# Kernel optimization log

Measured on AMD Instinct MI355X. Metric: run time of the kernel, lower is better.

Reference implementation:

```python
import jax, jax.numpy as jnp
import numpy as np

K = 5            # trend_kernel_size
PAD = K // 2
EPS = 1e-5

def _ricker(k):
    # Ricker (mexican-hat) wavelet used as the Peaks kernel
    a = k / 4.0
    t = np.arange(k, dtype=np.float64) - (k - 1) / 2.0
    A = 2.0 / (np.sqrt(3.0 * a) * np.pi ** 0.25)
    return (A * (1.0 - (t / a) ** 2) * np.exp(-t ** 2 / (2.0 * a ** 2))).astype(np.float32)

def _ramp(k):
    # centered linear ramp -> local slope estimator for the Trend kernel
    return (np.linspace(-1.0, 1.0, k) / k).astype(np.float32)

_PEAK_W = jnp.asarray(_ricker(K))
_RAMP_W = jnp.asarray(_ramp(K))

def tconv(x, w):
    # 'same'-padded cross-correlation along the time axis (axis=2) of (B,C,T,H,W)
    T = x.shape[2]
    xp = jnp.pad(x, ((0, 0), (0, 0), (PAD, PAD), (0, 0), (0, 0)))
    out = w[0] * jax.lax.dynamic_slice_in_dim(xp, 0, T, axis=2)
    for j in range(1, K):
        out = out + w[j] * jax.lax.dynamic_slice_in_dim(xp, j, T, axis=2)
    return out

def bn(x, gamma, beta, axes):
    # training-mode batch norm over `axes`, channel axis = 1
    m = x.mean(axes, keepdims=True)
    v = x.var(axes, keepdims=True)
    xn = (x - m) * jax.lax.rsqrt(v + EPS)
    shp = [1] * x.ndim
    shp[1] = -1
    return xn * gamma.reshape(shp) + beta.reshape(shp)


def setup_inputs() -> dict:
    key = jax.random.key(0)
    ks = jax.random.split(key, 8)
    B, C, T, H, W = 4, 3, 12, 256, 256
    CH0 = 32
    return {
        'x':      jax.random.normal(ks[0], (B, C, T, H, W), jnp.float32),
        'w0':     jax.random.normal(ks[1], (CH0, C), jnp.float32) * 0.1,
        'g0':     jnp.ones((CH0,), jnp.float32),
        'b0':     jnp.zeros((CH0,), jnp.float32),
        'wrt':    jax.random.normal(ks[2], (1, CH0), jnp.float32) * 0.1,
        'grt':    jnp.ones((1,), jnp.float32),
        'brt':    jnp.zeros((1,), jnp.float32),
        'wtt':    jax.random.normal(ks[3], (1, C), jnp.float32) * 0.1,
        'gtt':    jnp.ones((1,), jnp.float32),
        'btt':    jnp.zeros((1,), jnp.float32),
        'w_th':   jax.random.normal(ks[4], (CH0, T), jnp.float32) * 0.1,
        'b_th':   jnp.zeros((CH0,), jnp.float32),
        'g_min':  jnp.ones((CH0,), jnp.float32),
        'b_min':  jnp.zeros((CH0,), jnp.float32),
        'g_max':  jnp.ones((CH0,), jnp.float32),
        'b_max':  jnp.zeros((CH0,), jnp.float32),
        'g_mean': jnp.ones((CH0,), jnp.float32),
        'b_mean': jnp.zeros((CH0,), jnp.float32),
    }


def reference(x, w0, g0, b0, wrt, grt, brt, wtt, gtt, btt,
              w_th, b_th, g_min, b_min, g_max, b_max, g_mean, b_mean):
    act = jax.nn.silu
    # --- per-band temporal kernels (vectorized over all bands/pixels) ---
    peak = tconv(x, _PEAK_W)                       # Peaks: ricker wavelet
    slope = tconv(x, _RAMP_W)                      # Trend: local slope
    trend = peak + jax.nn.relu(slope) + jax.nn.relu(-slope)  # (B,C,T,H,W)
    # --- time_conv0: 1x1x1 conv3d + BN3d + act ---
    h = act(bn(jnp.einsum('bcthw,oc->bothw', x, w0), g0, b0, (0, 2, 3, 4)))  # (B,32,T,H,W)
    # --- reduce_to_time / reduce_trend_to_time: 1x1x1 conv3d to 1 channel ---
    rt = act(bn(jnp.einsum('bcthw,oc->bothw', h, wrt), grt, brt, (0, 2, 3, 4)))[:, 0]      # (B,T,H,W)
    tt = act(bn(jnp.einsum('bcthw,oc->bothw', trend, wtt), gtt, btt, (0, 2, 3, 4)))[:, 0]  # (B,T,H,W)
    # --- time_to_hidden: 1x1 conv2d over the time-as-channels axis ---
    time_logits = jnp.einsum('bthw,ot->bohw', rt + tt, w_th) + b_th[None, :, None, None]
    # --- channel reductions over time + BN2d + act (mean branch uses max, as in source) ---
    xmin = h.min(axis=2)
    xmax = h.max(axis=2)
    cmin = act(bn(xmin, g_min, b_min, (0, 2, 3)))
    cmax = act(bn(xmax, g_max, b_max, (0, 2, 3)))
    cmean = act(bn(xmax, g_mean, b_mean, (0, 2, 3)))
    enc = time_logits + cmin + cmax + cmean        # (B,32,H,W)
    # --- InstanceNorm2d(affine=False) ---
    m = enc.mean((2, 3), keepdims=True)
    v = enc.var((2, 3), keepdims=True)
    return (enc - m) * jax.lax.rsqrt(v + EPS)
```

## Files before the change

kernel.cpp:

```cpp
#include <hip/hip_runtime.h>
#include <math.h>

#define HW_    65536
#define THW_   786432
#define NP     262144
#define N1_    3145728.0
#define N3_    262144.0

#define XB 0
#define SB 72
#define EB 1128
#define DWN 2152

__device__ __constant__ float PW_[5] = {-0.33647654f, 0.20279402f, 0.77575913f, 0.20279402f, -0.33647654f};
__device__ __constant__ float RW_[5] = {-0.2f, -0.1f, 0.0f, 0.1f, 0.2f};

typedef __fp16 fp16x2 __attribute__((ext_vector_type(2)));
union H2U { fp16x2 h; unsigned int u; };
__device__ __forceinline__ unsigned int packh(float a, float b) {
  H2U x; x.h = __builtin_amdgcn_cvt_pkrtz(a, b); return x.u;
}
__device__ __forceinline__ float2 unpackh(unsigned int v) {
  H2U x; x.u = v; return make_float2((float)x.h.x, (float)x.h.y);
}
__device__ __forceinline__ unsigned short pack1h(float a) {
  return (unsigned short)(packh(a, 0.f) & 0xffffu);
}

__device__ __forceinline__ float wred64(float v) {
#pragma unroll
  for (int m = 32; m > 0; m >>= 1) v += __shfl_xor(v, m, 64);
  return v;
}

__device__ __forceinline__ float fsilu(float y) {
  float e = __expf(-y);
  return y * __builtin_amdgcn_rcpf(1.0f + e);
}

__global__ __launch_bounds__(256) void k_xstats(const float* __restrict__ x, double* __restrict__ dws) {
  const int v = blockIdx.x * 256 + threadIdx.x;
  const float4* x4 = (const float4*)x;
  float s0 = 0, s1 = 0, s2 = 0, p00 = 0, p01 = 0, p02 = 0, p11 = 0, p12 = 0, p22 = 0;
#pragma unroll
  for (int b = 0; b < 4; b++) {
    float4 a0 = x4[(size_t)(b * 3 + 0) * 196608 + v];
    float4 a1 = x4[(size_t)(b * 3 + 1) * 196608 + v];
    float4 a2 = x4[(size_t)(b * 3 + 2) * 196608 + v];
    s0 += a0.x + a0.y + a0.z + a0.w;
    s1 += a1.x + a1.y + a1.z + a1.w;
    s2 += a2.x + a2.y + a2.z + a2.w;
    p00 += a0.x * a0.x + a0.y * a0.y + a0.z * a0.z + a0.w * a0.w;
    p11 += a1.x * a1.x + a1.y * a1.y + a1.z * a1.z + a1.w * a1.w;
    p22 += a2.x * a2.x + a2.y * a2.y + a2.z * a2.z + a2.w * a2.w;
    p01 += a0.x * a1.x + a0.y * a1.y + a0.z * a1.z + a0.w * a1.w;
    p02 += a0.x * a2.x + a0.y * a2.y + a0.z * a2.z + a0.w * a2.w;
    p12 += a1.x * a2.x + a1.y * a2.y + a1.z * a2.z + a1.w * a2.w;
  }
  float vals[9] = {s0, s1, s2, p00, p01, p02, p11, p12, p22};
  __shared__ float red[4][9];
  int wave = threadIdx.x >> 6, lane = threadIdx.x & 63;
#pragma unroll
  for (int q = 0; q < 9; q++) vals[q] = wred64(vals[q]);
  if (lane == 0) {
#pragma unroll
    for (int q = 0; q < 9; q++) red[wave][q] = vals[q];
  }
  __syncthreads();
  if (threadIdx.x < 9) {
    double t = (double)red[0][threadIdx.x] + red[1][threadIdx.x] + red[2][threadIdx.x] + red[3][threadIdx.x];
    atomicAdd(&dws[XB + threadIdx.x * 8 + (blockIdx.x & 7)], t);
  }
}

__global__ __launch_bounds__(256) void k_passB(const float* __restrict__ x, const float* __restrict__ wrt,
                                               const float* __restrict__ wtt, const float* __restrict__ w0,
                                               const float* __restrict__ g0, const float* __restrict__ b0,
                                               unsigned int* __restrict__ pRT, unsigned int* __restrict__ pMM,
                                               double* __restrict__ dws) {
  const int tid = threadIdx.x;
  const int pix = blockIdx.x * 256 + tid;
  const int b = pix >> 16, hw = pix & 65535;
  __shared__ unsigned int lmm[32 * 264];
  __shared__ float red[4][4];
  __shared__ float cfa0[32], cfa1[32], cfa2[32], cfb[32];

  if (tid < 32) {
    int o = tid;
    double q[9];
#pragma unroll
    for (int i = 0; i < 9; i++) {
      double t = 0;
#pragma unroll
      for (int s = 0; s < 8; s++) t += dws[XB + i * 8 + s];
      q[i] = t / N1_;
    }
    double c0 = w0[o * 3 + 0], c1 = w0[o * 3 + 1], c2 = w0[o * 3 + 2];
    double Ey = c0 * q[0] + c1 * q[1] + c2 * q[2];
    double Ey2 = c0 * c0 * q[3] + c1 * c1 * q[6] + c2 * c2 * q[8] +
                 2.0 * (c0 * c1 * q[4] + c0 * c2 * q[5] + c1 * c2 * q[7]);
    double var = Ey2 - Ey * Ey;
    double alpha = (double)g0[o] / sqrt(var + 1e-5);
    cfa0[o] = (float)(alpha * c0);
    cfa1[o] = (float)(alpha * c1);
    cfa2[o] = (float)(alpha * c2);
    cfb[o]  = (float)((double)b0[o] - Ey * alpha);
  }
  __syncthreads();

  const float* xp = x + (size_t)b * 3 * THW_ + hw;
  float xv[3][12];
#pragma unroll
  for (int c = 0; c < 3; c++)
#pragma unroll
    for (int t = 0; t < 12; t++) xv[c][t] = xp[(size_t)(c * 12 + t) * HW_];
  float wt[3] = {wtt[0], wtt[1], wtt[2]};
  float ttp[12];
#pragma unroll
  for (int t = 0; t < 12; t++) {
    float acc = 0.f;
#pragma unroll
    for (int c = 0; c < 3; c++) {
      float pk = 0.f, sl = 0.f;
#pragma unroll
      for (int j = 0; j < 5; j++) {
        int tj = t - 2 + j;
        if (tj >= 0 && tj < 12) {
          pk = fmaf(PW_[j], xv[c][tj], pk);
          sl = fmaf(RW_[j], xv[c][tj], sl);
        }
      }
      acc = fmaf(wt[c], pk + fabsf(sl), acc);
    }
    ttp[t] = acc;
  }
  float rt_t[12];
#pragma unroll
  for (int t = 0; t < 12; t++) rt_t[t] = 0.f;
#pragma unroll
  for (int o = 0; o < 32; o++) {
    float a0 = cfa0[o], a1 = cfa1[o], a2 = cfa2[o];
    float bet = cfb[o], wo = wrt[o];
    float mn = 3.4e38f, mx = -3.4e38f;
#pragma unroll
    for (int t = 0; t < 12; t++) {
      float y = fmaf(a0, xv[0][t], fmaf(a1, xv[1][t], fmaf(a2, xv[2][t], bet)));
      float h = fsilu(y);
      mn = fminf(mn, h);
      mx = fmaxf(mx, h);
      rt_t[t] = fmaf(wo, h, rt_t[t]);
    }
    unsigned int pk = packh(mn, mx);
    pMM[o * NP + pix] = pk;
    lmm[o * 264 + tid] = pk;
  }
#pragma unroll
  for (int t = 0; t < 12; t++) pRT[t * NP + pix] = packh(rt_t[t], ttp[t]);

  {
    float srt = 0.f, ssrt = 0.f, stt = 0.f, sstt = 0.f;
#pragma unroll
    for (int t = 0; t < 12; t++) {
      srt += rt_t[t];  ssrt = fmaf(rt_t[t], rt_t[t], ssrt);
      stt += ttp[t];   sstt = fmaf(ttp[t], ttp[t], sstt);
    }
    srt = wred64(srt); ssrt = wred64(ssrt); stt = wred64(stt); sstt = wred64(sstt);
    int wave = tid >> 6, lane = tid & 63;
    if (lane == 0) { red[wave][0] = srt; red[wave][1] = ssrt; red[wave][2] = stt; red[wave][3] = sstt; }
  }
  __syncthreads();
  if (tid < 4) {
    double v = (double)red[0][tid] + red[1][tid] + red[2][tid] + red[3][tid];
    atomicAdd(&dws[SB + (128 + tid) * 8 + (blockIdx.x & 7)], v);
  }
  {
    int o = tid >> 3, j = tid & 7;
    float smn = 0, smn2 = 0, smx = 0, smx2 = 0;
#pragma unroll
    for (int k = 0; k < 32; k++) {
      float2 mm = unpackh(lmm[o * 264 + j + k * 8]);
      smn += mm.x; smn2 = fmaf(mm.x, mm.x, smn2);
      smx += mm.y; smx2 = fmaf(mm.y, mm.y, smx2);
    }
#pragma unroll
    for (int m = 1; m < 8; m <<= 1) {
      smn  += __shfl_xor(smn, m, 64);
      smn2 += __shfl_xor(smn2, m, 64);
      smx  += __shfl_xor(smx, m, 64);
      smx2 += __shfl_xor(smx2, m, 64);
    }
    if (j == 0) {
      int sh = blockIdx.x & 7;
      atomicAdd(&dws[SB + (o * 4 + 0) * 8 + sh], (double)smn);
      atomicAdd(&dws[SB + (o * 4 + 1) * 8 + sh], (double)smn2);
      atomicAdd(&dws[SB + (o * 4 + 2) * 8 + sh], (double)smx);
      atomicAdd(&dws[SB + (o * 4 + 3) * 8 + sh], (double)smx2);
    }
  }
}

template<bool FP16OUT>
__global__ __launch_bounds__(256) void k_passC(const unsigned int* __restrict__ pRT,
                                               const unsigned int* __restrict__ pMM,
                                               const float* __restrict__ wth, const float* __restrict__ bth,
                                               const float* __restrict__ grt, const float* __restrict__ brt,
                                               const float* __restrict__ gtt, const float* __restrict__ btt,
                                               const float* __restrict__ gmin, const float* __restrict__ bmin,
                                               const float* __restrict__ gmax, const float* __restrict__ bmax,
                                               const float* __restrict__ gmean, const float* __restrict__ bmean,
                                               const double* __restrict__ dws, float* __restrict__ out,
                                               unsigned short* __restrict__ penc) {
  const int tid = threadIdx.x;
  const int pix = blockIdx.x * 256 + tid;
  const int b = pix >> 16, hw = pix & 65535;
  __shared__ float camn[32], cbmn[32], camx[32], cbmx[32], came[32], cbme[32];
  __shared__ float c4[4];

  if (tid < 32) {
    double q[4];
#pragma unroll
    for (int i = 0; i < 4; i++) {
      double t = 0;
#pragma unroll
      for (int s = 0; s < 8; s++) t += dws[SB + (tid * 4 + i) * 8 + s];
      q[i] = t / N3_;
    }
    double m = q[0], v = q[1] - m * m;
    double a = (double)gmin[tid] / sqrt(v + 1e-5);
    camn[tid] = (float)a; cbmn[tid] = (float)((double)bmin[tid] - m * a);
    double mm = q[2], vv = q[3] - mm * mm;
    a = (double)gmax[tid] / sqrt(vv + 1e-5);
    camx[tid] = (float)a; cbmx[tid] = (float)((double)bmax[tid] - mm * a);
    a = (double)gmean[tid] / sqrt(vv + 1e-5);
    came[tid] = (float)a; cbme[tid] = (float)((double)bmean[tid] - mm * a);
  }
  if (tid == 32) {
    double q[4];
#pragma unroll
    for (int i = 0; i < 4; i++) {
      double t = 0;
#pragma unroll
      for (int s = 0; s < 8; s++) t += dws[SB + (128 + i) * 8 + s];
      q[i] = t / N1_;
    }
    double m = q[0], v = q[1] - m * m;
    double a = (double)grt[0] / sqrt(v + 1e-5);
    c4[0] = (float)a; c4[1] = (float)((double)brt[0] - m * a);
    m = q[2]; v = q[3] - m * m;
    a = (double)gtt[0] / sqrt(v + 1e-5);
    c4[2] = (float)a; c4[3] = (float)((double)btt[0] - m * a);
  }
  __syncthreads();

  float art = c4[0], brt_ = c4[1], att = c4[2], btt_ = c4[3];
  float rtt[12];
#pragma unroll
  for (int t = 0; t < 12; t++) {
    float2 v = unpackh(pRT[t * NP + pix]);
    rtt[t] = fsilu(fmaf(art, v.x, brt_)) + fsilu(fmaf(att, v.y, btt_));
  }
  float* po = out + (size_t)b * 32 * HW_ + hw;
  unsigned short* pe = penc + ((size_t)(b * 32) << 16) + hw;
#pragma unroll
  for (int o = 0; o < 32; o++) {
    float2 mm = unpackh(pMM[o * NP + pix]);
    float tl = bth[o];
#pragma unroll
    for (int t = 0; t < 12; t++) tl = fmaf(wth[o * 12 + t], rtt[t], tl);
    float e = tl + fsilu(fmaf(camn[o], mm.x, cbmn[o]))
                 + fsilu(fmaf(camx[o], mm.y, cbmx[o]))
                 + fsilu(fmaf(came[o], mm.y, cbme[o]));
    if (FP16OUT) pe[(size_t)o << 16] = pack1h(e);
    else         po[(size_t)o * HW_] = e;
  }
}

__global__ __launch_bounds__(256) void k_encstats16(const unsigned short* __restrict__ penc,
                                                    double* __restrict__ dws) {
  __shared__ float red[4][2];
  int s = blockIdx.x >> 1, sub = blockIdx.x & 1, tid = threadIdx.x;
  const uint4* p = (const uint4*)(penc + ((size_t)s << 16));
  float S = 0, SS = 0;
#pragma unroll 4
  for (int it = 0; it < 16; it++) {
    uint4 v = p[sub * 4096 + tid + it * 256];
    float2 a = unpackh(v.x), b = unpackh(v.y), c = unpackh(v.z), d = unpackh(v.w);
    S += a.x + a.y + b.x + b.y + c.x + c.y + d.x + d.y;
    SS += a.x * a.x + a.y * a.y + b.x * b.x + b.y * b.y +
          c.x * c.x + c.y * c.y + d.x * d.x + d.y * d.y;
  }
  S = wred64(S); SS = wred64(SS);
  int wave = tid >> 6, lane = tid & 63;
  if (lane == 0) { red[wave][0] = S; red[wave][1] = SS; }
  __syncthreads();
  if (tid < 2) {
    double v = (double)red[0][tid] + red[1][tid] + red[2][tid] + red[3][tid];
    atomicAdd(&dws[EB + (s * 2 + tid) * 4 + sub], v);
  }
}

__global__ __launch_bounds__(256) void k_inorm16(const double* __restrict__ dws,
                                                 const unsigned short* __restrict__ penc,
                                                 float* __restrict__ out) {
  int s = blockIdx.y;
  double S = 0, SS = 0;
#pragma unroll
  for (int sh = 0; sh < 4; sh++) {
    S  += dws[EB + (s * 2 + 0) * 4 + sh];
    SS += dws[EB + (s * 2 + 1) * 4 + sh];
  }
  double m = S / 65536.0, v = SS / 65536.0 - m * m;
  float rstd = (float)(1.0 / sqrt(v + 1e-5));
  float mf = (float)m;
  const uint2* p = (const uint2*)(penc + ((size_t)s << 16));
  float4* po = (float4*)(out + ((size_t)s << 16));
  int i = blockIdx.x * 256 + threadIdx.x;
  uint2 u = p[i];
  float2 a = unpackh(u.x), b = unpackh(u.y);
  float4 r;
  r.x = (a.x - mf) * rstd;
  r.y = (a.y - mf) * rstd;
  r.z = (b.x - mf) * rstd;
  r.w = (b.y - mf) * rstd;
  po[i] = r;
}

__global__ __launch_bounds__(256) void k_encstats32(const float* __restrict__ out, double* __restrict__ dws) {
  __shared__ float red[4][2];
  int s = blockIdx.x >> 2, sub = blockIdx.x & 3, tid = threadIdx.x;
  const float4* p = (const float4*)(out + ((size_t)s << 16));
  float S = 0, SS = 0;
#pragma unroll 4
  for (int it = 0; it < 16; it++) {
    float4 a = p[sub * 256 + tid + it * 1024];
    S += a.x + a.y + a.z + a.w;
    SS += a.x * a.x + a.y * a.y + a.z * a.z + a.w * a.w;
  }
  S = wred64(S); SS = wred64(SS);
  int wave = tid >> 6, lane = tid & 63;
  if (lane == 0) { red[wave][0] = S; red[wave][1] = SS; }
  __syncthreads();
  if (tid < 2) {
    double v = (double)red[0][tid] + red[1][tid] + red[2][tid] + red[3][tid];
    atomicAdd(&dws[EB + (s * 2 + tid) * 4 + sub], v);
  }
}

__global__ __launch_bounds__(256) void k_inorm32(const double* __restrict__ dws, float* __restrict__ out) {
  int s = blockIdx.y;
  double S = 0, SS = 0;
#pragma unroll
  for (int sh = 0; sh < 4; sh++) {
    S  += dws[EB + (s * 2 + 0) * 4 + sh];
    SS += dws[EB + (s * 2 + 1) * 4 + sh];
  }
  double m = S / 65536.0, v = SS / 65536.0 - m * m;
  float rstd = (float)(1.0 / sqrt(v + 1e-5));
  float mf = (float)m;
  float4* p = (float4*)(out + ((size_t)s << 16));
  int i = blockIdx.x * 256 + threadIdx.x;
  float4 a = p[i];
  a.x = (a.x - mf) * rstd;
  a.y = (a.y - mf) * rstd;
  a.z = (a.z - mf) * rstd;
  a.w = (a.w - mf) * rstd;
  p[i] = a;
}

extern "C" void kernel_launch(void* const* d_in, const int* in_sizes, int n_in,
                              void* d_out, int out_size, void* d_ws, size_t ws_size,
                              hipStream_t stream) {
  const float* x     = (const float*)d_in[0];
  const float* w0    = (const float*)d_in[1];
  const float* g0    = (const float*)d_in[2];
  const float* b0    = (const float*)d_in[3];
  const float* wrt   = (const float*)d_in[4];
  const float* grt   = (const float*)d_in[5];
  const float* brt   = (const float*)d_in[6];
  const float* gtt   = (const float*)d_in[8];
  const float* wtt   = (const float*)d_in[7];
  const float* btt   = (const float*)d_in[9];
  const float* wth   = (const float*)d_in[10];
  const float* bth   = (const float*)d_in[11];
  const float* gmin  = (const float*)d_in[12];
  const float* bmin  = (const float*)d_in[13];
  const float* gmax  = (const float*)d_in[14];
  const float* bmax  = (const float*)d_in[15];
  const float* gmean = (const float*)d_in[16];
  const float* bmean = (const float*)d_in[17];
  double* dws = (double*)d_ws;
  unsigned int* pRT = (unsigned int*)((char*)d_ws + 65536);
  unsigned int* pMM = pRT + 12 * NP;
  unsigned short* pENC = (unsigned short*)(pMM + 32 * NP);
  const size_t need16 = 65536 + (size_t)12 * NP * 4 + (size_t)32 * NP * 4 + (size_t)32 * NP * 2;
  const bool big = ws_size >= need16;
  float* out = (float*)d_out;

  hipMemsetAsync(d_ws, 0, DWN * sizeof(double), stream);
  hipLaunchKernelGGL(k_xstats, dim3(768), dim3(256), 0, stream, x, dws);
  hipLaunchKernelGGL(k_passB, dim3(1024), dim3(256), 0, stream, x, wrt, wtt, w0, g0, b0, pRT, pMM, dws);
  if (big) {
    hipLaunchKernelGGL((k_passC<true>), dim3(1024), dim3(256), 0, stream, pRT, pMM, wth, bth,
                       grt, brt, gtt, btt, gmin, bmin, gmax, bmax, gmean, bmean, dws, out, pENC);
    hipLaunchKernelGGL(k_encstats16, dim3(256), dim3(256), 0, stream, pENC, dws);
    hipLaunchKernelGGL(k_inorm16, dim3(64, 128), dim3(256), 0, stream, dws, pENC, out);
  } else {
    hipLaunchKernelGGL((k_passC<false>), dim3(1024), dim3(256), 0, stream, pRT, pMM, wth, bth,
                       grt, brt, gtt, btt, gmin, bmin, gmax, bmax, gmean, bmean, dws, out, pENC);
    hipLaunchKernelGGL(k_encstats32, dim3(512), dim3(256), 0, stream, out, dws);
    hipLaunchKernelGGL(k_inorm32, dim3(64, 128), dim3(256), 0, stream, dws, out);
  }
}
```

Before: 113.3 us.

## Split min/max stats out of passB and widen grids for stats kernels

Removes the large LDS staging buffer and in-block min/max statistics reduction from k_passB and computes those statistics in a separate k_stats kernel that re-reads pMM from global memory. k_xstats is launched with four times as many blocks, one per batch, and k_encstats16 with twice as many blocks, both aimed at more parallelism and more memory requests in flight. Freeing the LDS buffer may raise passB occupancy, but the new kernel re-reads 32 MB of packed min/max data and adds a launch, plus more double atomics.

```diff
diff --git a/kernel.cpp b/kernel.cpp
--- a/kernel.cpp
+++ b/kernel.cpp
@@ -39,24 +39,21 @@
 }
 
 __global__ __launch_bounds__(256) void k_xstats(const float* __restrict__ x, double* __restrict__ dws) {
-  const int v = blockIdx.x * 256 + threadIdx.x;
+  const int b = blockIdx.x & 3;
+  const int v = (blockIdx.x >> 2) * 256 + threadIdx.x;
   const float4* x4 = (const float4*)x;
-  float s0 = 0, s1 = 0, s2 = 0, p00 = 0, p01 = 0, p02 = 0, p11 = 0, p12 = 0, p22 = 0;
-#pragma unroll
-  for (int b = 0; b < 4; b++) {
-    float4 a0 = x4[(size_t)(b * 3 + 0) * 196608 + v];
-    float4 a1 = x4[(size_t)(b * 3 + 1) * 196608 + v];
-    float4 a2 = x4[(size_t)(b * 3 + 2) * 196608 + v];
-    s0 += a0.x + a0.y + a0.z + a0.w;
-    s1 += a1.x + a1.y + a1.z + a1.w;
-    s2 += a2.x + a2.y + a2.z + a2.w;
-    p00 += a0.x * a0.x + a0.y * a0.y + a0.z * a0.z + a0.w * a0.w;
-    p11 += a1.x * a1.x + a1.y * a1.y + a1.z * a1.z + a1.w * a1.w;
-    p22 += a2.x * a2.x + a2.y * a2.y + a2.z * a2.z + a2.w * a2.w;
-    p01 += a0.x * a1.x + a0.y * a1.y + a0.z * a1.z + a0.w * a1.w;
-    p02 += a0.x * a2.x + a0.y * a2.y + a0.z * a2.z + a0.w * a2.w;
-    p12 += a1.x * a2.x + a1.y * a2.y + a1.z * a2.z + a1.w * a2.w;
-  }
+  float4 a0 = x4[(size_t)(b * 3 + 0) * 196608 + v];
+  float4 a1 = x4[(size_t)(b * 3 + 1) * 196608 + v];
+  float4 a2 = x4[(size_t)(b * 3 + 2) * 196608 + v];
+  float s0 = a0.x + a0.y + a0.z + a0.w;
+  float s1 = a1.x + a1.y + a1.z + a1.w;
+  float s2 = a2.x + a2.y + a2.z + a2.w;
+  float p00 = a0.x * a0.x + a0.y * a0.y + a0.z * a0.z + a0.w * a0.w;
+  float p11 = a1.x * a1.x + a1.y * a1.y + a1.z * a1.z + a1.w * a1.w;
+  float p22 = a2.x * a2.x + a2.y * a2.y + a2.z * a2.z + a2.w * a2.w;
+  float p01 = a0.x * a1.x + a0.y * a1.y + a0.z * a1.z + a0.w * a1.w;
+  float p02 = a0.x * a2.x + a0.y * a2.y + a0.z * a2.z + a0.w * a2.w;
+  float p12 = a1.x * a2.x + a1.y * a2.y + a1.z * a2.z + a1.w * a2.w;
   float vals[9] = {s0, s1, s2, p00, p01, p02, p11, p12, p22};
   __shared__ float red[4][9];
   int wave = threadIdx.x >> 6, lane = threadIdx.x & 63;
@@ -81,7 +78,6 @@
   const int tid = threadIdx.x;
   const int pix = blockIdx.x * 256 + tid;
   const int b = pix >> 16, hw = pix & 65535;
-  __shared__ unsigned int lmm[32 * 264];
   __shared__ float red[4][4];
   __shared__ float cfa0[32], cfa1[32], cfa2[32], cfb[32];
 
@@ -150,9 +146,7 @@
       mx = fmaxf(mx, h);
       rt_t[t] = fmaf(wo, h, rt_t[t]);
     }
-    unsigned int pk = packh(mn, mx);
-    pMM[o * NP + pix] = pk;
-    lmm[o * 264 + tid] = pk;
+    pMM[o * NP + pix] = packh(mn, mx);
   }
 #pragma unroll
   for (int t = 0; t < 12; t++) pRT[t * NP + pix] = packh(rt_t[t], ttp[t]);
@@ -173,29 +167,31 @@
     double v = (double)red[0][tid] + red[1][tid] + red[2][tid] + red[3][tid];
     atomicAdd(&dws[SB + (128 + tid) * 8 + (blockIdx.x & 7)], v);
   }
-  {
-    int o = tid >> 3, j = tid & 7;
-    float smn = 0, smn2 = 0, smx = 0, smx2 = 0;
-#pragma unroll
-    for (int k = 0; k < 32; k++) {
-      float2 mm = unpackh(lmm[o * 264 + j + k * 8]);
-      smn += mm.x; smn2 = fmaf(mm.x, mm.x, smn2);
-      smx += mm.y; smx2 = fmaf(mm.y, mm.y, smx2);
-    }
-#pragma unroll
-    for (int m = 1; m < 8; m <<= 1) {
-      smn  += __shfl_xor(smn, m, 64);
-      smn2 += __shfl_xor(smn2, m, 64);
-      smx  += __shfl_xor(smx, m, 64);
-      smx2 += __shfl_xor(smx2, m, 64);
-    }
-    if (j == 0) {
-      int sh = blockIdx.x & 7;
-      atomicAdd(&dws[SB + (o * 4 + 0) * 8 + sh], (double)smn);
-      atomicAdd(&dws[SB + (o * 4 + 1) * 8 + sh], (double)smn2);
-      atomicAdd(&dws[SB + (o * 4 + 2) * 8 + sh], (double)smx);
-      atomicAdd(&dws[SB + (o * 4 + 3) * 8 + sh], (double)smx2);
-    }
+}
+
+__global__ __launch_bounds__(256) void k_stats(const unsigned int* __restrict__ pMM,
+                                               double* __restrict__ dws) {
+  __shared__ float red[4][4];
+  int o = blockIdx.x >> 5, sub = blockIdx.x & 31, tid = threadIdx.x;
+  const uint4* p = (const uint4*)(pMM + (size_t)o * NP);
+  int base = sub * 256 + tid;
+  float s0 = 0, s1 = 0, s2 = 0, s3 = 0;
+#pragma unroll
+  for (int it = 0; it < 8; it++) {
+    uint4 v = p[base + it * 8192];
+    float2 a = unpackh(v.x), b = unpackh(v.y), c = unpackh(v.z), d = unpackh(v.w);
+    s0 += a.x + b.x + c.x + d.x;
+    s1 += a.x * a.x + b.x * b.x + c.x * c.x + d.x * d.x;
+    s2 += a.y + b.y + c.y + d.y;
+    s3 += a.y * a.y + b.y * b.y + c.y * c.y + d.y * d.y;
+  }
+  s0 = wred64(s0); s1 = wred64(s1); s2 = wred64(s2); s3 = wred64(s3);
+  int wave = tid >> 6, lane = tid & 63;
+  if (lane == 0) { red[wave][0] = s0; red[wave][1] = s1; red[wave][2] = s2; red[wave][3] = s3; }
+  __syncthreads();
+  if (tid < 4) {
+    double v = (double)red[0][tid] + red[1][tid] + red[2][tid] + red[3][tid];
+    atomicAdd(&dws[SB + (o * 4 + tid) * 8 + (blockIdx.x & 7)], v);
   }
 }
 
@@ -278,12 +274,12 @@
 __global__ __launch_bounds__(256) void k_encstats16(const unsigned short* __restrict__ penc,
                                                     double* __restrict__ dws) {
   __shared__ float red[4][2];
-  int s = blockIdx.x >> 1, sub = blockIdx.x & 1, tid = threadIdx.x;
+  int s = blockIdx.x >> 2, sub = blockIdx.x & 3, tid = threadIdx.x;
   const uint4* p = (const uint4*)(penc + ((size_t)s << 16));
   float S = 0, SS = 0;
-#pragma unroll 4
-  for (int it = 0; it < 16; it++) {
-    uint4 v = p[sub * 4096 + tid + it * 256];
+#pragma unroll
+  for (int it = 0; it < 8; it++) {
+    uint4 v = p[sub * 2048 + tid + it * 256];
     float2 a = unpackh(v.x), b = unpackh(v.y), c = unpackh(v.z), d = unpackh(v.w);
     S += a.x + a.y + b.x + b.y + c.x + c.y + d.x + d.y;
     SS += a.x * a.x + a.y * a.y + b.x * b.x + b.y * b.y +
@@ -377,8 +373,8 @@
   const float* wrt   = (const float*)d_in[4];
   const float* grt   = (const float*)d_in[5];
   const float* brt   = (const float*)d_in[6];
+  const float* wtt   = (const float*)d_in[7];
   const float* gtt   = (const float*)d_in[8];
-  const float* wtt   = (const float*)d_in[7];
   const float* btt   = (const float*)d_in[9];
   const float* wth   = (const float*)d_in[10];
   const float* bth   = (const float*)d_in[11];
@@ -397,12 +393,13 @@
   float* out = (float*)d_out;
 
   hipMemsetAsync(d_ws, 0, DWN * sizeof(double), stream);
-  hipLaunchKernelGGL(k_xstats, dim3(768), dim3(256), 0, stream, x, dws);
+  hipLaunchKernelGGL(k_xstats, dim3(3072), dim3(256), 0, stream, x, dws);
   hipLaunchKernelGGL(k_passB, dim3(1024), dim3(256), 0, stream, x, wrt, wtt, w0, g0, b0, pRT, pMM, dws);
+  hipLaunchKernelGGL(k_stats, dim3(1024), dim3(256), 0, stream, pMM, dws);
   if (big) {
     hipLaunchKernelGGL((k_passC<true>), dim3(1024), dim3(256), 0, stream, pRT, pMM, wth, bth,
                        grt, brt, gtt, btt, gmin, bmin, gmax, bmax, gmean, bmean, dws, out, pENC);
-    hipLaunchKernelGGL(k_encstats16, dim3(256), dim3(256), 0, stream, pENC, dws);
+    hipLaunchKernelGGL(k_encstats16, dim3(512), dim3(256), 0, stream, pENC, dws);
     hipLaunchKernelGGL(k_inorm16, dim3(64, 128), dim3(256), 0, stream, dws, pENC, out);
   } else {
     hipLaunchKernelGGL((k_passC<false>), dim3(1024), dim3(256), 0, stream, pRT, pMM, wth, bth,
```

New measurement: 164.9 us. 45.6% more time.
